# Performance work log

Hardware: AMD Instinct MI355X
Metric: run time of the kernel (lower is better)

Reference implementation:

```python
import jax, jax.numpy as jnp
import numpy as np

K_CLASSES = 5   # num support classes (5-way)
N_SHOT = 5      # supports per class


def setup_inputs() -> dict:
    key = jax.random.key(0)
    k0, k1, k2, k3 = jax.random.split(key, 4)
    b, bs, c, h, w = 32, K_CLASSES * N_SHOT, 512, 14, 14
    dk, dv = 128, 128
    return {
        "support_features": jax.random.normal(k0, (bs, c, h, w), jnp.float32),
        "query_features": jax.random.normal(k1, (b, c, h, w), jnp.float32),
        "support_labels": jnp.repeat(jnp.arange(K_CLASSES), N_SHOT).astype(jnp.int32),
        "W_qk": jax.random.normal(k2, (dk, c), jnp.float32) * 0.02,  # 1x1 conv weight
        "W_v": jax.random.normal(k3, (dv, c), jnp.float32) * 0.02,   # 1x1 conv weight
    }


def reference(support_features, query_features, support_labels, W_qk, W_v):
    scale = 1.0  # 1/temperature, temperature=1.0
    # 1x1 convs == channel-mixing einsums
    query_q = jnp.einsum('bchw,dc->bdhw', query_features, W_qk)
    query_v = jnp.einsum('bchw,dc->bdhw', query_features, W_v)
    supp_k = jnp.einsum('nchw,dc->ndhw', support_features, W_qk)
    supp_v = jnpveinsum = jnp.einsum('nchw,dc->ndhw', support_features, W_v)
    supp_v = jnpveinsum
    b, cv, h, w = query_v.shape

    # similarity over all supports: [b,h,w,n,i,j] (contracts dim_key)
    sim = jnp.einsum('bchw,ncij->bhwnij', query_q, supp_k) * scale

    # per-class masked softmax over the (n,i,j) axes restricted to that class's
    # supports == index_select + softmax in the original loop (labels balanced).
    cls_mask = support_labels[None, :] == jnp.arange(K_CLASSES)[:, None]  # [K,n]
    neg = jnp.finfo(sim.dtype).min
    sim_k = jnp.where(cls_mask[:, None, None, None, :, None, None], sim[None], neg)  # [K,b,h,w,n,i,j]
    attn = jax.nn.softmax(sim_k.reshape(K_CLASSES, b, h, w, -1), axis=-1)
    attn = attn.reshape(sim_k.shape)  # masked-out entries -> exactly 0

    # weighted sum of support values: [K,b,c,h,w]
    out = jnp.einsum('kbhwnij,ncij->kbchw', attn, supp_v)
    prototypes = jnp.transpose(out, (1, 0, 2, 3, 4)).reshape(b, K_CLASSES, -1)  # b k (c h w)
    query_v_flat = query_v.reshape(b, 1, -1)  # b () (c h w)
    return prototypes, query_v_flat
```

## Files before the change

### kernel.cpp

```cpp
#include <hip/hip_runtime.h>
#include <cstdint>
#include <cstddef>

#define NB   32
#define NSUP 25
#define KCLS 5
#define NC   512
#define ND   128
#define NP   196
#define JS   208
#define SHIFT 8.0f

#define KPITCH 272
#define KTILE  (16 * KPITCH)
#define KBUF   (2 * KTILE)
#define VPITCH 80
#define VBUF   (128 * VPITCH)
#define BUFSZ  (KBUF + VBUF)

#define NGRP   (NB * KCLS * 13)
#define PACC_F ((size_t)NGRP * 2 * 2048)
#define PSUM_F ((size_t)NGRP * 2 * 16)

typedef __attribute__((ext_vector_type(8))) short short8;
typedef __attribute__((ext_vector_type(4))) float floatx4;

__device__ inline short f2bf(float x) {
  union { float f; uint32_t u; } v; v.f = x;
  uint32_t r = (v.u + 0x7FFFu + ((v.u >> 16) & 1u)) >> 16;
  return (short)(r & 0xFFFFu);
}
__device__ inline uint32_t pk2(float a, float b) {
  return (uint32_t)(uint16_t)f2bf(a) | ((uint32_t)(uint16_t)f2bf(b) << 16);
}

__global__ __launch_bounds__(256) void wconv_kernel(
    const float* __restrict__ Wqk, const float* __restrict__ Wv,
    uint16_t* __restrict__ Whi)
{
  const int f = (blockIdx.x * 256 + (int)threadIdx.x) * 8;
  const float* src = (f < ND * NC) ? (Wqk + f) : (Wv + f - ND * NC);
  short8 hv;
  #pragma unroll
  for (int i = 0; i < 8; ++i) hv[i] = f2bf(src[i]);
  *(short8*)(Whi + f) = hv;
}

__global__ __launch_bounds__(256) void gemm_kernel(
    const float* __restrict__ supp, const float* __restrict__ qry,
    const uint16_t* __restrict__ Whi,
    uint16_t* __restrict__ Qt, uint16_t* __restrict__ Kt,
    uint16_t* __restrict__ Vt, float* __restrict__ outVq)
{
  __shared__ uint16_t xs[16 * 520];
  const int bx = blockIdx.x;
  const int t16 = bx % 13, img = bx / 13;
  const int tid = (int)threadIdx.x;
  const int w = tid >> 6, lane = tid & 63, ln = lane & 15, q = lane >> 4;
  const int d0 = w * 32;
  const int p0 = t16 * 16;

  const float* __restrict__ X = (img < NB)
      ? (qry  + (size_t)img * NC * NP)
      : (supp + (size_t)(img - NB) * NC * NP);

  #pragma unroll
  for (int k = 0; k < 4; ++k) {
    const int id = k * 256 + tid;
    const int cp = id >> 2;
    const int pq = id & 3;
    int pg = p0 + pq * 4; if (pg > NP - 4) pg = NP - 4;
    const floatx4 fa = *(const floatx4*)(X + (2 * cp) * NP + pg);
    const floatx4 fb = *(const floatx4*)(X + (2 * cp + 1) * NP + pg);
    #pragma unroll
    for (int i = 0; i < 4; ++i)
      *((uint32_t*)xs + (pq * 4 + i) * 260 + cp) = pk2(fa[i], fb[i]);
  }
  __syncthreads();

  floatx4 aQ[2], aV[2];
  #pragma unroll
  for (int nt = 0; nt < 2; ++nt) {
    aQ[nt] = (floatx4){0.f, 0.f, 0.f, 0.f};
    aV[nt] = (floatx4){0.f, 0.f, 0.f, 0.f};
  }

  for (int ks = 0; ks < 16; ++ks) {
    const short8 xh = *(const short8*)&xs[ln * 520 + ks * 32 + q * 8];
    #pragma unroll
    for (int nt = 0; nt < 2; ++nt) {
      const size_t wr = (size_t)(d0 + nt * 16 + ln) * NC + ks * 32 + q * 8;
      const short8 wqh = *(const short8*)(Whi + wr);
      aQ[nt] = __builtin_amdgcn_mfma_f32_16x16x32_bf16(xh, wqh, aQ[nt], 0, 0, 0);
      const short8 wvh = *(const short8*)(Whi + (size_t)ND * NC + wr);
      aV[nt] = __builtin_amdgcn_mfma_f32_16x16x32_bf16(wvh, xh, aV[nt], 0, 0, 0);
    }
  }

  if (img < NB) {
    #pragma unroll
    for (int nt = 0; nt < 2; ++nt)
      #pragma unroll
      for (int rr = 0; rr < 4; ++rr) {
        const int p = p0 + q * 4 + rr;
        if (p < NP)
          Qt[((size_t)img * NP + p) * ND + d0 + nt * 16 + ln] = (uint16_t)f2bf(aQ[nt][rr]);
      }
  } else {
    const int n = img - NB;
    #pragma unroll
    for (int nt = 0; nt < 2; ++nt)
      #pragma unroll
      for (int rr = 0; rr < 4; ++rr) {
        const int p = p0 + q * 4 + rr;
        Kt[((size_t)n * JS + p) * ND + d0 + nt * 16 + ln] = (uint16_t)f2bf(aQ[nt][rr]);
      }
  }
  const int p = p0 + ln;
  if (img < NB) {
    if (p < NP) {
      #pragma unroll
      for (int nt = 0; nt < 2; ++nt)
        #pragma unroll
        for (int rr = 0; rr < 4; ++rr)
          outVq[((size_t)img * ND + d0 + nt * 16 + q * 4 + rr) * NP + p] = aV[nt][rr];
    }
  } else {
    const int n = img - NB;
    #pragma unroll
    for (int nt = 0; nt < 2; ++nt)
      #pragma unroll
      for (int rr = 0; rr < 4; ++rr)
        Vt[((size_t)n * ND + d0 + nt * 16 + q * 4 + rr) * JS + p] = (uint16_t)f2bf(aV[nt][rr]);
  }
}

template <int NCHUNK, bool PART>
__global__ __launch_bounds__(256, 2) void attn_kernel(
    const uint16_t* __restrict__ Qt, const uint16_t* __restrict__ Kt,
    const uint16_t* __restrict__ Vt, const int* __restrict__ labels,
    float* __restrict__ out, float* __restrict__ pacc, float* __restrict__ psum)
{
  __shared__ __align__(16) char smem[2 * BUFSZ];

  const int bx = blockIdx.x;
  const int pt = bx % 13;
  const int rem = bx / 13;
  const int kc = rem % KCLS;
  const int rest = rem / KCLS;
  const int bq = PART ? (rest & 7) : rest;
  const int half = PART ? (rest >> 3) : 0;
  const int c0 = half * NCHUNK;
  const int b0 = bq * 4;
  const int p0 = pt * 16;
  const int tid = (int)threadIdx.x;
  const int w = tid >> 6, lane = tid & 63, ln = lane & 15, q = lane >> 4;
  const int b = b0 + w;

  const int myl = (lane < NSUP) ? labels[lane] : -1;
  unsigned long long m = __ballot(myl == kc);
  int clsPack = 0;
  #pragma unroll
  for (int s = 0; s < 5; ++s) {
    const int n = (m != 0ull) ? (int)__builtin_ctzll(m) : 0;
    clsPack |= n << (6 * s);
    m &= (m - 1);
  }

  short8 aq[4];
  {
    int p = p0 + ln; if (p > NP - 1) p = NP - 1;
    const uint16_t* base = Qt + ((size_t)b * NP + p) * ND + q * 8;
    #pragma unroll
    for (int ks = 0; ks < 4; ++ks) aq[ks] = *(const short8*)(base + ks * 32);
  }

  floatx4 acc[8];
  #pragma unroll
  for (int dt = 0; dt < 8; ++dt) acc[dt] = (floatx4){0.f, 0.f, 0.f, 0.f};
  float Ssum = 0.f;

  const int alo = (ln + ((q & 1) << 5)) << 2;
  const bool hiTile = (q >= 2);

  int4 pf[4];
  {
    int nk[2], j0k[2], nv[2], jv[2];
    #pragma unroll
    for (int t = 0; t < 2; ++t) {
      const int tile16 = c0 * 2 + t;
      int s = tile16 / 13;
      j0k[t] = (tile16 - s * 13) * 16;
      if (s > 4) s = 4;
      nk[t] = (clsPack >> (6 * s)) & 63;
    }
    #pragma unroll
    for (int h = 0; h < 2; ++h) {
      const int ch = c0 * 32 + h * 16;
      int sv = ch / JS, jvv = ch - sv * JS;
      if (sv > 4) { sv = 4; jvv = 192; }
      nv[h] = (clsPack >> (6 * sv)) & 63;
      jv[h] = jvv;
    }
    #pragma unroll
    for (int pass = 0; pass < 4; ++pass) {
      const int slot = pass * 256 + tid;
      if (pass < 2) {
        const int t = slot >> 8, r = (slot >> 4) & 15, sc = slot & 15;
        pf[pass] = *(const int4*)(Kt + ((size_t)(nk[t] * JS + j0k[t] + r)) * ND + sc * 8);
      } else {
        const int vs = slot - 512;
        const int h = vs >> 8, d = (vs >> 1) & 127, sc2 = vs & 1;
        pf[pass] = *(const int4*)(Vt + ((size_t)(nv[h] * ND + d)) * JS + jv[h] + sc2 * 8);
      }
    }
    char* db = smem;
    #pragma unroll
    for (int pass = 0; pass < 4; ++pass) {
      const int slot = pass * 256 + tid;
      if (pass < 2) {
        const int t = slot >> 8, r = (slot >> 4) & 15, sc = slot & 15;
        *(int4*)(db + t * KTILE + r * KPITCH + sc * 16) = pf[pass];
      } else {
        const int vs = slot - 512;
        const int h = vs >> 8, d = (vs >> 1) & 127, sc2 = vs & 1;
        *(int4*)(db + KBUF + d * VPITCH + (h * 2 + sc2) * 16) = pf[pass];
      }
    }
  }
  __syncthreads();

  for (int li = 0; li < NCHUNK; ++li) {
    const int cc = c0 + li;
    const int nc = cc + 1;
    int nk[2], j0k[2], nv[2], jv[2];
    if (li < NCHUNK - 1) {
      #pragma unroll
      for (int t = 0; t < 2; ++t) {
        const int tile16 = nc * 2 + t;
        int s = tile16 / 13;
        j0k[t] = (tile16 - s * 13) * 16;
        if (s > 4) s = 4;
        nk[t] = (clsPack >> (6 * s)) & 63;
      }
      #pragma unroll
      for (int h = 0; h < 2; ++h) {
        const int ch = nc * 32 + h * 16;
        int sv = ch / JS, jvv = ch - sv * JS;
        if (sv > 4) { sv = 4; jvv = 192; }
        nv[h] = (clsPack >> (6 * sv)) & 63;
        jv[h] = jvv;
      }
      #pragma unroll
      for (int pass = 0; pass < 4; ++pass) {
        const int slot = pass * 256 + tid;
        if (pass < 2) {
          const int t = slot >> 8, r = (slot >> 4) & 15, sc = slot & 15;
          pf[pass] = *(const int4*)(Kt + ((size_t)(nk[t] * JS + j0k[t] + r)) * ND + sc * 8);
        } else {
          const int vs = slot - 512;
          const int h = vs >> 8, d = (vs >> 1) & 127, sc2 = vs & 1;
          pf[pass] = *(const int4*)(Vt + ((size_t)(nv[h] * ND + d)) * JS + jv[h] + sc2 * 8);
        }
      }
    }

    const char* kb = smem + (li & 1) * BUFSZ;
    const char* vb = kb + KBUF;

    short8 av[8];
    #pragma unroll
    for (int dt = 0; dt < 8; ++dt)
      av[dt] = *(const short8*)(vb + (dt * 16 + ln) * VPITCH + q * 16);

    short8 bk[2][4];
    #pragma unroll
    for (int t = 0; t < 2; ++t)
      #pragma unroll
      for (int ks = 0; ks < 4; ++ks)
        bk[t][ks] = *(const short8*)(kb + t * KTILE + ln * KPITCH + ks * 64 + q * 16);

    floatx4 e0, e1;
    #pragma unroll
    for (int t = 0; t < 2; ++t) {
      const int tile16 = cc * 2 + t;
      const int s = tile16 / 13;
      const int j0 = (tile16 - s * 13) * 16;
      const bool tval = (s < 5);
      floatx4 d4 = {0.f, 0.f, 0.f, 0.f};
      #pragma unroll
      for (int ks = 0; ks < 4; ++ks)
        d4 = __builtin_amdgcn_mfma_f32_16x16x32_bf16(bk[t][ks], aq[ks], d4, 0, 0, 0);
      floatx4 ev;
      #pragma unroll
      for (int r = 0; r < 4; ++r) {
        const int j = j0 + q * 4 + r;
        const float e = (tval && j < NP) ? __expf(d4[r] - SHIFT) : 0.f;
        ev[r] = e;
        Ssum += e;
      }
      if (t == 0) e0 = ev; else e1 = ev;
    }

    short8 bp;
    #pragma unroll
    for (int r = 0; r < 4; ++r) {
      const uint32_t pe = pk2(e0[r], e1[r]);
      const int lo = __builtin_amdgcn_ds_bpermute(alo, (int)pe);
      const int hi = __builtin_amdgcn_ds_bpermute(alo + 64, (int)pe);
      bp[r]     = (short)(uint16_t)(hiTile ? (lo >> 16) : (lo & 0xFFFF));
      bp[4 + r] = (short)(uint16_t)(hiTile ? (hi >> 16) : (hi & 0xFFFF));
    }

    #pragma unroll
    for (int dt = 0; dt < 8; ++dt)
      acc[dt] = __builtin_amdgcn_mfma_f32_16x16x32_bf16(av[dt], bp, acc[dt], 0, 0, 0);

    if (li < NCHUNK - 1) {
      char* db = smem + ((li + 1) & 1) * BUFSZ;
      #pragma unroll
      for (int pass = 0; pass < 4; ++pass) {
        const int slot = pass * 256 + tid;
        if (pass < 2) {
          const int t = slot >> 8, r = (slot >> 4) & 15, sc = slot & 15;
          *(int4*)(db + t * KTILE + r * KPITCH + sc * 16) = pf[pass];
        } else {
          const int vs = slot - 512;
          const int h = vs >> 8, d = (vs >> 1) & 127, sc2 = vs & 1;
          *(int4*)(db + KBUF + d * VPITCH + (h * 2 + sc2) * 16) = pf[pass];
        }
      }
    }
    __syncthreads();
  }

  float sv = Ssum;
  sv += __shfl_xor(sv, 16);
  sv += __shfl_xor(sv, 32);

  if (PART) {
    const size_t grp = (((size_t)(b * KCLS + kc)) * 13 + pt) * 2 + half;
    float* pa = pacc + grp * 2048;
    #pragma unroll
    for (int dt = 0; dt < 8; ++dt)
      #pragma unroll
      for (int rr = 0; rr < 4; ++rr)
        pa[(dt * 16 + q * 4 + rr) * 16 + ln] = acc[dt][rr];
    if (q == 0) psum[grp * 16 + ln] = sv;
  } else {
    const float inv = 1.f / sv;
    const int pp = p0 + ln;
    if (pp < NP) {
      float* ob = out + ((size_t)(b * KCLS + kc) * ND + q * 4) * NP + pp;
      #pragma unroll
      for (int dt = 0; dt < 8; ++dt)
        #pragma unroll
        for (int rr = 0; rr < 4; ++rr)
          ob[(size_t)(dt * 16 + rr) * NP] = acc[dt][rr] * inv;
    }
  }
}

__global__ __launch_bounds__(256) void merge_kernel(
    const float* __restrict__ pacc, const float* __restrict__ psum,
    float* __restrict__ out)
{
  const int bx = blockIdx.x;
  const int pt = bx % 13;
  const int rem = bx / 13;
  const int tid = (int)threadIdx.x;
  const int ln = tid & 15, dr = tid >> 4;
  const size_t g0 = (((size_t)rem) * 13 + pt) * 2;

  const float s = psum[g0 * 16 + ln] + psum[(g0 + 1) * 16 + ln];
  const int pp = pt * 16 + ln;
  if (pp >= NP) return;
  const float inv = 1.f / s;

  const float* pa0 = pacc + g0 * 2048;
  const float* pa1 = pacc + (g0 + 1) * 2048;
  float* ob = out + (size_t)rem * ND * NP + pp;
  #pragma unroll
  for (int i = 0; i < 8; ++i) {
    const int d = dr * 8 + i;
    ob[(size_t)d * NP] = (pa0[d * 16 + ln] + pa1[d * 16 + ln]) * inv;
  }
}

extern "C" void kernel_launch(void* const* d_in, const int* in_sizes, int n_in,
                              void* d_out, int out_size, void* d_ws, size_t ws_size,
                              hipStream_t stream) {
  const float* supp   = (const float*)d_in[0];
  const float* qry    = (const float*)d_in[1];
  const int*   labels = (const int*)d_in[2];
  const float* Wqk    = (const float*)d_in[3];
  const float* Wv     = (const float*)d_in[4];
  float* out = (float*)d_out;

  uint16_t* Whi = (uint16_t*)d_ws;
  uint16_t* Qt  = Whi + (size_t)2 * ND * NC;
  uint16_t* Kt  = Qt  + (size_t)NB * NP * ND;
  uint16_t* Vt  = Kt  + (size_t)NSUP * JS * ND;
  float* pacc   = (float*)(Vt + (size_t)NSUP * ND * JS);
  float* psum   = pacc + PACC_F;
  const size_t need = (size_t)((char*)(psum + PSUM_F) - (char*)d_ws);
  float* outVq = out + (size_t)NB * KCLS * ND * NP;

  wconv_kernel<<<64, 256, 0, stream>>>(Wqk, Wv, Whi);
  gemm_kernel<<<741, 256, 0, stream>>>(supp, qry, Whi, Qt, Kt, Vt, outVq);
  if (ws_size >= need) {
    attn_kernel<17, true><<<1040, 256, 0, stream>>>(Qt, Kt, Vt, labels, out, pacc, psum);
    merge_kernel<<<2080, 256, 0, stream>>>(pacc, psum, out);
  } else {
    attn_kernel<33, false><<<520, 256, 0, stream>>>(Qt, Kt, Vt, labels, out, nullptr, nullptr);
  }
}
```

Before: 165.9 us.

## Process two queries per wavefront to reuse staged K/V tiles

Each wavefront now handles two batch queries instead of one, so a block covers eight queries and reuses the same shared-memory K and V tiles and fragments for both. This halves the grid size and the number of K/V staging passes per query. In exchange it doubles accumulator and Q-fragment registers, which may cut occupancy under the 2-blocks launch bound, and halves the number of blocks available to fill the GPU. The fallback path's chunk count also changes from 33 to 34.

```diff
diff --git a/kernel.cpp b/kernel.cpp
--- a/kernel.cpp
+++ b/kernel.cpp
@@ -148,14 +148,14 @@
   const int rem = bx / 13;
   const int kc = rem % KCLS;
   const int rest = rem / KCLS;
-  const int bq = PART ? (rest & 7) : rest;
-  const int half = PART ? (rest >> 3) : 0;
+  const int oct = PART ? (rest & 3) : rest;
+  const int half = PART ? (rest >> 2) : 0;
   const int c0 = half * NCHUNK;
-  const int b0 = bq * 4;
+  const int b0 = oct * 8;
   const int p0 = pt * 16;
   const int tid = (int)threadIdx.x;
   const int w = tid >> 6, lane = tid & 63, ln = lane & 15, q = lane >> 4;
-  const int b = b0 + w;
+  const int bA = b0 + w * 2, bB = bA + 1;
 
   const int myl = (lane < NSUP) ? labels[lane] : -1;
   unsigned long long m = __ballot(myl == kc);
@@ -167,18 +167,25 @@
     m &= (m - 1);
   }
 
-  short8 aq[4];
+  short8 aqA[4], aqB[4];
   {
     int p = p0 + ln; if (p > NP - 1) p = NP - 1;
-    const uint16_t* base = Qt + ((size_t)b * NP + p) * ND + q * 8;
-    #pragma unroll
-    for (int ks = 0; ks < 4; ++ks) aq[ks] = *(const short8*)(base + ks * 32);
-  }
-
-  floatx4 acc[8];
-  #pragma unroll
-  for (int dt = 0; dt < 8; ++dt) acc[dt] = (floatx4){0.f, 0.f, 0.f, 0.f};
-  float Ssum = 0.f;
+    const uint16_t* baseA = Qt + ((size_t)bA * NP + p) * ND + q * 8;
+    const uint16_t* baseB = Qt + ((size_t)bB * NP + p) * ND + q * 8;
+    #pragma unroll
+    for (int ks = 0; ks < 4; ++ks) {
+      aqA[ks] = *(const short8*)(baseA + ks * 32);
+      aqB[ks] = *(const short8*)(baseB + ks * 32);
+    }
+  }
+
+  floatx4 accA[8], accB[8];
+  #pragma unroll
+  for (int dt = 0; dt < 8; ++dt) {
+    accA[dt] = (floatx4){0.f, 0.f, 0.f, 0.f};
+    accB[dt] = (floatx4){0.f, 0.f, 0.f, 0.f};
+  }
+  float SsA = 0.f, SsB = 0.f;
 
   const int alo = (ln + ((q & 1) << 5)) << 2;
   const bool hiTile = (q >= 2);
@@ -280,41 +287,53 @@
       for (int ks = 0; ks < 4; ++ks)
         bk[t][ks] = *(const short8*)(kb + t * KTILE + ln * KPITCH + ks * 64 + q * 16);
 
-    floatx4 e0, e1;
+    floatx4 e0A, e1A, e0B, e1B;
     #pragma unroll
     for (int t = 0; t < 2; ++t) {
       const int tile16 = cc * 2 + t;
       const int s = tile16 / 13;
       const int j0 = (tile16 - s * 13) * 16;
       const bool tval = (s < 5);
-      floatx4 d4 = {0.f, 0.f, 0.f, 0.f};
-      #pragma unroll
-      for (int ks = 0; ks < 4; ++ks)
-        d4 = __builtin_amdgcn_mfma_f32_16x16x32_bf16(bk[t][ks], aq[ks], d4, 0, 0, 0);
-      floatx4 ev;
+      floatx4 d4A = {0.f, 0.f, 0.f, 0.f};
+      floatx4 d4B = {0.f, 0.f, 0.f, 0.f};
+      #pragma unroll
+      for (int ks = 0; ks < 4; ++ks) {
+        d4A = __builtin_amdgcn_mfma_f32_16x16x32_bf16(bk[t][ks], aqA[ks], d4A, 0, 0, 0);
+        d4B = __builtin_amdgcn_mfma_f32_16x16x32_bf16(bk[t][ks], aqB[ks], d4B, 0, 0, 0);
+      }
+      floatx4 evA, evB;
       #pragma unroll
       for (int r = 0; r < 4; ++r) {
         const int j = j0 + q * 4 + r;
-        const float e = (tval && j < NP) ? __expf(d4[r] - SHIFT) : 0.f;
-        ev[r] = e;
-        Ssum += e;
-      }
-      if (t == 0) e0 = ev; else e1 = ev;
-    }
-
-    short8 bp;
+        const bool val = (tval && j < NP);
+        const float eA = val ? __expf(d4A[r] - SHIFT) : 0.f;
+        const float eB = val ? __expf(d4B[r] - SHIFT) : 0.f;
+        evA[r] = eA; SsA += eA;
+        evB[r] = eB; SsB += eB;
+      }
+      if (t == 0) { e0A = evA; e0B = evB; } else { e1A = evA; e1B = evB; }
+    }
+
+    short8 bpA, bpB;
     #pragma unroll
     for (int r = 0; r < 4; ++r) {
-      const uint32_t pe = pk2(e0[r], e1[r]);
-      const int lo = __builtin_amdgcn_ds_bpermute(alo, (int)pe);
-      const int hi = __builtin_amdgcn_ds_bpermute(alo + 64, (int)pe);
-      bp[r]     = (short)(uint16_t)(hiTile ? (lo >> 16) : (lo & 0xFFFF));
-      bp[4 + r] = (short)(uint16_t)(hiTile ? (hi >> 16) : (hi & 0xFFFF));
-    }
-
-    #pragma unroll
-    for (int dt = 0; dt < 8; ++dt)
-      acc[dt] = __builtin_amdgcn_mfma_f32_16x16x32_bf16(av[dt], bp, acc[dt], 0, 0, 0);
+      const uint32_t peA = pk2(e0A[r], e1A[r]);
+      const int loA = __builtin_amdgcn_ds_bpermute(alo, (int)peA);
+      const int hiA = __builtin_amdgcn_ds_bpermute(alo + 64, (int)peA);
+      bpA[r]     = (short)(uint16_t)(hiTile ? (loA >> 16) : (loA & 0xFFFF));
+      bpA[4 + r] = (short)(uint16_t)(hiTile ? (hiA >> 16) : (hiA & 0xFFFF));
+      const uint32_t peB = pk2(e0B[r], e1B[r]);
+      const int loB = __builtin_amdgcn_ds_bpermute(alo, (int)peB);
+      const int hiB = __builtin_amdgcn_ds_bpermute(alo + 64, (int)peB);
+      bpB[r]     = (short)(uint16_t)(hiTile ? (loB >> 16) : (loB & 0xFFFF));
+      bpB[4 + r] = (short)(uint16_t)(hiTile ? (hiB >> 16) : (hiB & 0xFFFF));
+    }
+
+    #pragma unroll
+    for (int dt = 0; dt < 8; ++dt) {
+      accA[dt] = __builtin_amdgcn_mfma_f32_16x16x32_bf16(av[dt], bpA, accA[dt], 0, 0, 0);
+      accB[dt] = __builtin_amdgcn_mfma_f32_16x16x32_bf16(av[dt], bpB, accB[dt], 0, 0, 0);
+    }
 
     if (li < NCHUNK - 1) {
       char* db = smem + ((li + 1) & 1) * BUFSZ;
@@ -334,29 +353,42 @@
     __syncthreads();
   }
 
-  float sv = Ssum;
-  sv += __shfl_xor(sv, 16);
-  sv += __shfl_xor(sv, 32);
+  float svA = SsA;
+  svA += __shfl_xor(svA, 16);
+  svA += __shfl_xor(svA, 32);
+  float svB = SsB;
+  svB += __shfl_xor(svB, 16);
+  svB += __shfl_xor(svB, 32);
 
   if (PART) {
-    const size_t grp = (((size_t)(b * KCLS + kc)) * 13 + pt) * 2 + half;
-    float* pa = pacc + grp * 2048;
+    const size_t grpA = (((size_t)(bA * KCLS + kc)) * 13 + pt) * 2 + half;
+    const size_t grpB = (((size_t)(bB * KCLS + kc)) * 13 + pt) * 2 + half;
+    float* paA = pacc + grpA * 2048;
+    float* paB = pacc + grpB * 2048;
     #pragma unroll
     for (int dt = 0; dt < 8; ++dt)
       #pragma unroll
-      for (int rr = 0; rr < 4; ++rr)
-        pa[(dt * 16 + q * 4 + rr) * 16 + ln] = acc[dt][rr];
-    if (q == 0) psum[grp * 16 + ln] = sv;
+      for (int rr = 0; rr < 4; ++rr) {
+        paA[(dt * 16 + q * 4 + rr) * 16 + ln] = accA[dt][rr];
+        paB[(dt * 16 + q * 4 + rr) * 16 + ln] = accB[dt][rr];
+      }
+    if (q == 0) {
+      psum[grpA * 16 + ln] = svA;
+      psum[grpB * 16 + ln] = svB;
+    }
   } else {
-    const float inv = 1.f / sv;
     const int pp = p0 + ln;
     if (pp < NP) {
-      float* ob = out + ((size_t)(b * KCLS + kc) * ND + q * 4) * NP + pp;
+      const float invA = 1.f / svA, invB = 1.f / svB;
+      float* obA = out + ((size_t)(bA * KCLS + kc) * ND + q * 4) * NP + pp;
+      float* obB = out + ((size_t)(bB * KCLS + kc) * ND + q * 4) * NP + pp;
       #pragma unroll
       for (int dt = 0; dt < 8; ++dt)
         #pragma unroll
-        for (int rr = 0; rr < 4; ++rr)
-          ob[(size_t)(dt * 16 + rr) * NP] = acc[dt][rr] * inv;
+        for (int rr = 0; rr < 4; ++rr) {
+          obA[(size_t)(dt * 16 + rr) * NP] = accA[dt][rr] * invA;
+          obB[(size_t)(dt * 16 + rr) * NP] = accB[dt][rr] * invB;
+        }
     }
   }
 }
@@ -409,9 +441,9 @@
   wconv_kernel<<<64, 256, 0, stream>>>(Wqk, Wv, Whi);
   gemm_kernel<<<741, 256, 0, stream>>>(supp, qry, Whi, Qt, Kt, Vt, outVq);
   if (ws_size >= need) {
-    attn_kernel<17, true><<<1040, 256, 0, stream>>>(Qt, Kt, Vt, labels, out, pacc, psum);
+    attn_kernel<17, true><<<520, 256, 0, stream>>>(Qt, Kt, Vt, labels, out, pacc, psum);
     merge_kernel<<<2080, 256, 0, stream>>>(pacc, psum, out);
   } else {
-    attn_kernel<33, false><<<520, 256, 0, stream>>>(Qt, Kt, Vt, labels, out, nullptr, nullptr);
-  }
-}
+    attn_kernel<34, false><<<260, 256, 0, stream>>>(Qt, Kt, Vt, labels, out, nullptr, nullptr);
+  }
+}
```

Result: no change. 164.9 us (-0.6%).
